# Kernel optimization log

Measured on AMD Instinct MI355X. Metric: run time of the kernel, lower is better.

The kernel has to match this reference:

```python
import jax, jax.numpy as jnp
import numpy as np

B, T, C = 1, 2048, 1024
H, KVH = 16, 4
D = C // H            # 64
KV = KVH * D          # 256
EPS = 1e-6
SCALE = 1.0 / np.sqrt(D)
ROPE_BASE = 10000.0


def setup_inputs() -> dict:
    key = jax.random.key(0)
    ks = jax.random.split(key, 8)
    s = 0.02
    return dict(
        x=jax.random.normal(ks[0], (B, T, C), jnp.float32),
        Wq=jax.random.normal(ks[1], (C, C), jnp.float32) * s,
        Wk=jax.random.normal(ks[2], (KV, C), jnp.float32) * s,
        Wv=jax.random.normal(ks[3], (KV, C), jnp.float32) * s,
        Wo=jax.random.normal(ks[4], (C, C), jnp.float32) * s,
        q_norm_w=jnp.ones((C,), jnp.float32),
        k_norm_w=jnp.ones((KV,), jnp.float32),
        fgate_w=jax.random.normal(ks[5], (H, C), jnp.float32) * s,
        fgate_b=jnp.zeros((H,), jnp.float32),
        weight_lambda=jax.random.normal(ks[6], (C, H), jnp.float32) * s,
    )


def _rmsnorm(x, w):
    var = jnp.mean(x * x, axis=-1, keepdims=True)
    return x * jax.lax.rsqrt(var + EPS) * w


def _rotate_half(x):
    x1, x2 = jnp.split(x, 2, axis=-1)
    return jnp.concatenate([-x2, x1], axis=-1)


def _apply_rope(q, k):
    # q: [B,H,T,D], k: [B,KVH,T,D]; position_ids = arange(T)
    inv_freq = 1.0 / (ROPE_BASE ** (jnp.arange(0, D, 2, dtype=jnp.float32) / D))
    freqs = jnp.outer(jnp.arange(T, dtype=jnp.float32), inv_freq)  # [T, D/2]
    emb = jnp.concatenate([freqs, freqs], axis=-1)                 # [T, D]
    cos = jnp.cos(emb)[None, None]                                  # [1,1,T,D]
    sin = jnp.sin(emb)[None, None]
    return q * cos + _rotate_half(q) * sin, k * cos + _rotate_half(k) * sin


def _forward(x, Wq, Wk, Wv, Wo, q_norm_w, k_norm_w, fgate_w, fgate_b, weight_lambda):
    q = _rmsnorm(x @ Wq.T, q_norm_w)          # [B,T,C]
    k = _rmsnorm(x @ Wk.T, k_norm_w)          # [B,T,KV]
    v = x @ Wv.T                              # [B,T,KV]
    q = q.reshape(B, T, H, D).transpose(0, 2, 1, 3)     # [B,H,T,D]
    k = k.reshape(B, T, KVH, D).transpose(0, 2, 1, 3)   # [B,KVH,T,D]
    v = v.reshape(B, T, KVH, D).transpose(0, 2, 1, 3)
    q, k = _apply_rope(q, k)
    # GQA: repeat_interleave kv heads
    g = H // KVH
    k = jnp.repeat(k, g, axis=1)              # [B,H,T,D]
    v = jnp.repeat(v, g, axis=1)
    # Forgetting gate (FoX): log f_t per head, with elu-based lambda scaling
    lam = jax.nn.elu(x @ weight_lambda) + 1.0            # [B,T,H]
    logit = (x @ fgate_w.T + fgate_b) * lam              # [B,T,H]
    log_f = (jax.nn.log_sigmoid(logit) / (lam + 1e-3)).transpose(0, 2, 1)  # [B,H,T]
    c = jnp.cumsum(log_f, axis=-1)                       # [B,H,T]
    bias = c[..., :, None] - c[..., None, :]             # [B,H,T,T]: sum_{t=j+1..i} log f_t
    scores = jnp.einsum('bhid,bhjd->bhij', q, k) * SCALE + bias
    causal = jnp.tril(jnp.ones((T, T), dtype=bool))
    scores = jnp.where(causal, scores, -jnp.inf)
    p = jax.nn.softmax(scores, axis=-1)
    y = jnp.einsum('bhij,bhjd->bhid', p, v)              # [B,H,T,D]
    y = y.transpose(0, 2, 1, 3).reshape(B, T, C)
    return y @ Wo.T


def reference(x, Wq, Wk, Wv, Wo, q_norm_w, k_norm_w, fgate_w, fgate_b, weight_lambda):
    return _forward(x, Wq, Wk, Wv, Wo, q_norm_w, k_norm_w, fgate_w, fgate_b, weight_lambda)
```

## Files before the change

kernel.cpp:

```cpp
#include <hip/hip_runtime.h>

typedef __bf16 bf16x8 __attribute__((ext_vector_type(8)));
typedef float f32x4 __attribute__((ext_vector_type(4)));

#define MFMA_BF16 __builtin_amdgcn_mfma_f32_16x16x32_bf16

static constexpr int T_ = 2048;
static constexpr int C_ = 1024;
static constexpr int H_ = 16;
static constexpr int KVH_ = 4;
static constexpr int D_ = 64;
static constexpr float INVLN2_ = 1.4426950408889634f;
static constexpr float SCALE2_ = 0.125f * 1.4426950408889634f;
static constexpr float MSHIFT_ = 10.0f;

static constexpr int UPH_ = 528;
static constexpr int NBLK_ = 1024;

__device__ inline void cvt8(__bf16* dst, const float* src) {
  float4 a = *(const float4*)src;
  float4 b = *(const float4*)(src + 4);
  bf16x8 r;
  r[0] = (__bf16)a.x; r[1] = (__bf16)a.y; r[2] = (__bf16)a.z; r[3] = (__bf16)a.w;
  r[4] = (__bf16)b.x; r[5] = (__bf16)b.y; r[6] = (__bf16)b.z; r[7] = (__bf16)b.w;
  *(bf16x8*)dst = r;
}

__global__ __launch_bounds__(256) void cvt_kernel(
    const float* __restrict__ x,  const float* __restrict__ wq,
    const float* __restrict__ wk, const float* __restrict__ wv,
    const float* __restrict__ wo, const float* __restrict__ wl,
    __bf16* __restrict__ xb,  __bf16* __restrict__ wqb,
    __bf16* __restrict__ wkb, __bf16* __restrict__ wvb,
    __bf16* __restrict__ wob, float* __restrict__ wlT,
    float* __restrict__ zbuf)
{
  size_t i8 = ((size_t)blockIdx.x * 256 + threadIdx.x) * 8;
  if (i8 < 2097152)       cvt8(xb  + i8,            x  + i8);
  else if (i8 < 3145728)  cvt8(wqb + (i8-2097152),  wq + (i8-2097152));
  else if (i8 < 3407872)  cvt8(wkb + (i8-3145728),  wk + (i8-3145728));
  else if (i8 < 3670016)  cvt8(wvb + (i8-3407872),  wv + (i8-3407872));
  else if (i8 < 4718592)  cvt8(wob + (i8-3670016),  wo + (i8-3670016));
  else if (i8 < 4734976) {
    size_t r = i8 - 4718592;
#pragma unroll
    for (int j = 0; j < 8; ++j) {
      size_t idx = r + j;
      size_t hh = idx >> 10, c = idx & 1023;
      wlT[idx] = wl[c * 16 + hh];
    }
  } else {
    size_t z = i8 - 4734976;
    if (z < 2129920) {
      float4 zz = {0.f, 0.f, 0.f, 0.f};
      *(float4*)(zbuf + z) = zz;
      *(float4*)(zbuf + z + 4) = zz;
    }
  }
}

template <int BM>
__global__ __launch_bounds__(256) void gemm_bt_kernel(
    const __bf16* __restrict__ A, int K, int N,
    const __bf16* __restrict__ B0, int e0,
    const __bf16* __restrict__ B1, int e1,
    const __bf16* __restrict__ B2,
    float* __restrict__ outF)
{
  __shared__ __bf16 la[BM * 40];
  __shared__ __bf16 lb[128 * 40];
  const int m0 = blockIdx.y * BM;
  const int n0 = blockIdx.x * 128;
  const __bf16* Bs; int nrel;
  if (n0 < e0)      { Bs = B0; nrel = n0; }
  else if (n0 < e1) { Bs = B1; nrel = n0 - e0; }
  else              { Bs = B2; nrel = n0 - e1; }
  const int tid = threadIdx.x;
  const int arow = tid >> 2, acol = (tid & 3) * 8;
  const __bf16* ap = A  + (size_t)(m0   + arow) * K + acol;
  const __bf16* bp = Bs + (size_t)(nrel + arow) * K + acol;
  const int w = tid >> 6, lane = tid & 63, lq = lane >> 4, ln = lane & 15;
  const int wm = (w >> 1) * (BM / 2), wn = (w & 1) * 64;
  constexpr int FM = BM / 32;
  f32x4 acc[FM][4] = {};
  for (int k0 = 0; k0 < K; k0 += 32) {
    bf16x8 a0 = *(const bf16x8*)(ap + k0);
    bf16x8 a1{};
    if (BM == 128) a1 = *(const bf16x8*)(ap + (size_t)64 * K + k0);
    bf16x8 b0 = *(const bf16x8*)(bp + k0);
    bf16x8 b1 = *(const bf16x8*)(bp + (size_t)64 * K + k0);
    __syncthreads();
    *(bf16x8*)(la + arow * 40 + acol) = a0;
    if (BM == 128) *(bf16x8*)(la + (arow + 64) * 40 + acol) = a1;
    *(bf16x8*)(lb + arow * 40 + acol) = b0;
    *(bf16x8*)(lb + (arow + 64) * 40 + acol) = b1;
    __syncthreads();
    bf16x8 af[FM], bfr[4];
#pragma unroll
    for (int i = 0; i < FM; ++i)
      af[i] = *(const bf16x8*)(la + (wm + i * 16 + ln) * 40 + lq * 8);
#pragma unroll
    for (int j = 0; j < 4; ++j)
      bfr[j] = *(const bf16x8*)(lb + (wn + j * 16 + ln) * 40 + lq * 8);
#pragma unroll
    for (int i = 0; i < FM; ++i)
#pragma unroll
      for (int j = 0; j < 4; ++j)
        acc[i][j] = MFMA_BF16(af[i], bfr[j], acc[i][j], 0, 0, 0);
  }
#pragma unroll
  for (int i = 0; i < FM; ++i)
#pragma unroll
    for (int j = 0; j < 4; ++j)
#pragma unroll
      for (int r = 0; r < 4; ++r) {
        int row = m0 + wm + i * 16 + lq * 4 + r;
        int col = n0 + wn + j * 16 + ln;
        outF[(size_t)row * N + col] = acc[i][j][r];
      }
}

__global__ __launch_bounds__(256) void gemmout_kernel(
    const float* __restrict__ oacc, const float* __restrict__ lsacc,
    const __bf16* __restrict__ B, float* __restrict__ outF)
{
  constexpr int K = 1024, N = 1024;
  __shared__ __bf16 la[64 * 40];
  __shared__ __bf16 lb[128 * 40];
  const int m0 = blockIdx.y * 64;
  const int n0 = blockIdx.x * 128;
  const int tid = threadIdx.x;
  const int arow = tid >> 2, acol = (tid & 3) * 8;
  const int trow = m0 + arow;
  const __bf16* bp = B + (size_t)(n0 + arow) * K + acol;
  const int w = tid >> 6, lane = tid & 63, lq = lane >> 4, ln = lane & 15;
  const int wm = (w >> 1) * 32, wn = (w & 1) * 64;
  f32x4 acc[2][4] = {};
  for (int k0 = 0; k0 < K; k0 += 32) {
    const int c = k0 + acol;
    const int hh = c >> 6, d = c & 63;
    const float* op = oacc + ((size_t)hh * T_ + trow) * D_ + d;
    float4 f0 = *(const float4*)(op);
    float4 f1 = *(const float4*)(op + 4);
    float inv = __builtin_amdgcn_rcpf(lsacc[(size_t)hh * T_ + trow]);
    bf16x8 a0;
    a0[0] = (__bf16)(f0.x * inv); a0[1] = (__bf16)(f0.y * inv);
    a0[2] = (__bf16)(f0.z * inv); a0[3] = (__bf16)(f0.w * inv);
    a0[4] = (__bf16)(f1.x * inv); a0[5] = (__bf16)(f1.y * inv);
    a0[6] = (__bf16)(f1.z * inv); a0[7] = (__bf16)(f1.w * inv);
    bf16x8 b0 = *(const bf16x8*)(bp + k0);
    bf16x8 b1 = *(const bf16x8*)(bp + (size_t)64 * K + k0);
    __syncthreads();
    *(bf16x8*)(la + arow * 40 + acol) = a0;
    *(bf16x8*)(lb + arow * 40 + acol) = b0;
    *(bf16x8*)(lb + (arow + 64) * 40 + acol) = b1;
    __syncthreads();
    bf16x8 af[2], bfr[4];
#pragma unroll
    for (int i = 0; i < 2; ++i)
      af[i] = *(const bf16x8*)(la + (wm + i * 16 + ln) * 40 + lq * 8);
#pragma unroll
    for (int j = 0; j < 4; ++j)
      bfr[j] = *(const bf16x8*)(lb + (wn + j * 16 + ln) * 40 + lq * 8);
#pragma unroll
    for (int i = 0; i < 2; ++i)
#pragma unroll
      for (int j = 0; j < 4; ++j)
        acc[i][j] = MFMA_BF16(af[i], bfr[j], acc[i][j], 0, 0, 0);
  }
#pragma unroll
  for (int i = 0; i < 2; ++i)
#pragma unroll
    for (int j = 0; j < 4; ++j)
#pragma unroll
      for (int r = 0; r < 4; ++r) {
        int row = m0 + wm + i * 16 + lq * 4 + r;
        int col = n0 + wn + j * 16 + ln;
        outF[(size_t)row * N + col] = acc[i][j][r];
      }
}

__global__ __launch_bounds__(256) void gates_kernel(
    const float* __restrict__ x, const float* __restrict__ fw,
    const float* __restrict__ fb, const float* __restrict__ wlT,
    float* __restrict__ logf)
{
  const int t0 = blockIdx.x * 4;
  const int tid = threadIdx.x, w = tid >> 6, lane = tid & 63;
  float xv[4][16];
#pragma unroll
  for (int tt = 0; tt < 4; ++tt)
#pragma unroll
    for (int i = 0; i < 16; ++i)
      xv[tt][i] = x[(size_t)(t0 + tt) * C_ + i * 64 + lane];
#pragma unroll
  for (int u = 0; u < 4; ++u) {
    int h = w * 4 + u;
    float wlr[16], fwr[16];
#pragma unroll
    for (int i = 0; i < 16; ++i) {
      wlr[i] = wlT[(size_t)h * C_ + i * 64 + lane];
      fwr[i] = fw[(size_t)h * C_ + i * 64 + lane];
    }
#pragma unroll
    for (int tt = 0; tt < 4; ++tt) {
      float s1 = 0.f, s2 = 0.f;
#pragma unroll
      for (int i = 0; i < 16; ++i) {
        s1 += xv[tt][i] * wlr[i];
        s2 += xv[tt][i] * fwr[i];
      }
      for (int m = 32; m; m >>= 1) {
        s1 += __shfl_xor(s1, m);
        s2 += __shfl_xor(s2, m);
      }
      if (lane == 0) {
        float lam = (s1 > 0.f ? s1 : expm1f(s1)) + 1.0f;
        float logit = (s2 + fb[h]) * lam;
        float ls = (logit >= 0.f) ? -log1pf(expf(-logit))
                                  : (logit - log1pf(expf(logit)));
        logf[(size_t)h * T_ + t0 + tt] = ls / (lam + 1e-3f);
      }
    }
  }
}

__global__ __launch_bounds__(256) void cumsum_kernel(
    const float* __restrict__ logf, float* __restrict__ csum)
{
  const int h = blockIdx.x;
  const int tid = threadIdx.x, lane = tid & 63, w = tid >> 6;
  __shared__ float wsum[4];
  const float* src = logf + (size_t)h * T_ + tid * 8;
  float4 a = *(const float4*)(src);
  float4 b = *(const float4*)(src + 4);
  float v[8] = {a.x, a.y, a.z, a.w, b.x, b.y, b.z, b.w};
  float t = 0.f;
#pragma unroll
  for (int j = 0; j < 8; ++j) t += v[j];
  float s = t;
#pragma unroll
  for (int d = 1; d < 64; d <<= 1) {
    float u = __shfl_up(s, d);
    if (lane >= d) s += u;
  }
  if (lane == 63) wsum[w] = s;
  __syncthreads();
  float prefix = 0.f;
#pragma unroll
  for (int ww = 0; ww < 3; ++ww)
    if (ww < w) prefix += wsum[ww];
  float run = prefix + s - t;
  float* dst = csum + (size_t)h * T_ + tid * 8;
  float4 o0, o1;
  run += v[0]; o0.x = run; run += v[1]; o0.y = run;
  run += v[2]; o0.z = run; run += v[3]; o0.w = run;
  run += v[4]; o1.x = run; run += v[5]; o1.y = run;
  run += v[6]; o1.z = run; run += v[7]; o1.w = run;
  *(float4*)dst = o0;
  *(float4*)(dst + 4) = o1;
}

__global__ __launch_bounds__(256) void normrope_kernel(
    const float* __restrict__ qkv, const float* __restrict__ qw,
    const float* __restrict__ kw, __bf16* __restrict__ qh,
    __bf16* __restrict__ kh, __bf16* __restrict__ vh)
{
  const int t = blockIdx.x, tid = threadIdx.x;
  __shared__ float qn[1024];
  __shared__ float kn[256];
  __shared__ float red[16];
  __shared__ float rc[32], rs[32];
  if (tid < 32) {
    float fr = (float)t * exp2f((float)tid * -0.41524101186404527f);
    float sn, cs;
    sincosf(fr, &sn, &cs);
    rc[tid] = cs; rs[tid] = sn;
  }
  const float* row = qkv + (size_t)t * 1536;
  float4 q4 = *(const float4*)(row + tid * 4);
  float kvl = row[1024 + tid];
  float vvl = row[1280 + tid];
  float ssq = q4.x * q4.x + q4.y * q4.y + q4.z * q4.z + q4.w * q4.w;
  float ssk = kvl * kvl;
  const int lane = tid & 63, w = tid >> 6;
  for (int m = 32; m; m >>= 1) {
    ssq += __shfl_xor(ssq, m);
    ssk += __shfl_xor(ssk, m);
  }
  if (lane == 0) { red[w] = ssq; red[8 + w] = ssk; }
  __syncthreads();
  float sq = red[0] + red[1] + red[2] + red[3];
  float sk = red[8] + red[9] + red[10] + red[11];
  float rq = rsqrtf(sq * (1.0f / 1024.f) + 1e-6f);
  float rk = rsqrtf(sk * (1.0f / 256.f) + 1e-6f);
  qn[tid * 4 + 0] = q4.x * rq * qw[tid * 4 + 0];
  qn[tid * 4 + 1] = q4.y * rq * qw[tid * 4 + 1];
  qn[tid * 4 + 2] = q4.z * rq * qw[tid * 4 + 2];
  qn[tid * 4 + 3] = q4.w * rq * qw[tid * 4 + 3];
  kn[tid] = kvl * rk * kw[tid];
  __syncthreads();
#pragma unroll
  for (int u = 0; u < 4; ++u) {
    int cidx = tid * 4 + u;
    int hh = cidx >> 6, d = cidx & 63, i = d & 31;
    float cs = rc[i], sn = rs[i];
    float val = (d < 32) ? (qn[cidx] * cs - qn[cidx + 32] * sn)
                         : (qn[cidx] * cs + qn[cidx - 32] * sn);
    qh[(size_t)hh * T_ * D_ + (size_t)t * D_ + d] = (__bf16)val;
  }
  {
    int d = tid & 63, kvhh = tid >> 6, i = d & 31;
    float cs = rc[i], sn = rs[i];
    float kval = (d < 32) ? (kn[tid] * cs - kn[tid + 32] * sn)
                          : (kn[tid] * cs + kn[tid - 32] * sn);
    kh[(size_t)kvhh * T_ * D_ + (size_t)t * D_ + d] = (__bf16)kval;
    vh[(size_t)kvhh * T_ * D_ + (size_t)t * D_ + d] = (__bf16)vvl;
  }
}

__global__ __launch_bounds__(256) void vtrans_kernel(
    const __bf16* __restrict__ vh, __bf16* __restrict__ vt)
{
  const int tb = blockIdx.x, kvh = blockIdx.y;
  __shared__ __bf16 tile[64][72];
  const int tid = threadIdx.x;
  const int r = tid >> 2, cb = (tid & 3) * 16;
  const __bf16* src = vh + (size_t)kvh * T_ * D_ + (size_t)(tb * 64 + r) * D_ + cb;
  bf16x8 v0 = *(const bf16x8*)(src);
  bf16x8 v1 = *(const bf16x8*)(src + 8);
  *(bf16x8*)(&tile[r][cb]) = v0;
  *(bf16x8*)(&tile[r][cb + 8]) = v1;
  __syncthreads();
  bf16x8 o0, o1;
#pragma unroll
  for (int j = 0; j < 8; ++j) o0[j] = tile[cb + j][r];
#pragma unroll
  for (int j = 0; j < 8; ++j) o1[j] = tile[cb + 8 + j][r];
  __bf16* dst = vt + (size_t)kvh * D_ * T_ + (size_t)r * T_ + tb * 64 + cb;
  *(bf16x8*)(dst) = o0;
  *(bf16x8*)(dst + 8) = o1;
}

__device__ inline unsigned cvtpk_bf16(float a, float b) {
  unsigned r;
  asm("v_cvt_pk_bf16_f32 %0, %1, %2" : "=v"(r) : "v"(a), "v"(b));
  return r;
}

__global__ __launch_bounds__(256, 4) void attn_kernel(
    const __bf16* __restrict__ qh, const __bf16* __restrict__ kh,
    const __bf16* __restrict__ vt, const float* __restrict__ csum,
    float* __restrict__ oacc, float* __restrict__ lsacc)
{
  const int bid = blockIdx.x;
  const int wgid = (bid & 7) * (NBLK_ / 8) + (bid >> 3);
  const int g4 = wgid >> 2, r4 = wgid & 3;
  const int u0 = g4 * 33 + (r4 ? 9 + (r4 - 1) * 8 : 0);
  const int cnt = r4 ? 8 : 9;
  __shared__ __bf16 kbuf[2][64 * 72];
  __shared__ __bf16 vbuf[2][64 * 72];
  const int tid = threadIdx.x;
  const int w = tid >> 6, lane = tid & 63, lq = lane >> 4, ln = lane & 15;
  const int srow = tid >> 2, scol = (tid & 3) * 16;
  bf16x8 ones;
#pragma unroll
  for (int j = 0; j < 8; ++j) ones[j] = (__bf16)1.0f;

  auto dec = [](int u, int& h, int& ib, int& jt) {
    h = u / UPH_;
    int uh = u - h * UPH_;
    int b = (int)((sqrtf((float)(8 * uh + 1)) - 1.f) * 0.5f);
    if (b * (b + 1) / 2 > uh) --b;
    if ((b + 1) * (b + 2) / 2 <= uh) ++b;
    ib = b; jt = uh - b * (b + 1) / 2;
  };

  int h, ib, jt;
  dec(u0, h, ib, jt);
  int kvh = h >> 2;

  bf16x8 aq0, aq1;
  float ci2;
  f32x4 o[4] = {};
  f32x4 ls = {0.f, 0.f, 0.f, 0.f};
  auto loadQ = [&](int h_, int i0_) {
    const __bf16* qp = qh + ((size_t)h_ * T_ + i0_ + w * 16 + ln) * D_;
    aq0 = *(const bf16x8*)(qp + lq * 8);
    aq1 = *(const bf16x8*)(qp + 32 + lq * 8);
    ci2 = (csum[(size_t)h_ * T_ + i0_ + w * 16 + ln] - MSHIFT_) * INVLN2_;
#pragma unroll
    for (int dd = 0; dd < 4; ++dd) o[dd] = f32x4{0.f, 0.f, 0.f, 0.f};
    ls = f32x4{0.f, 0.f, 0.f, 0.f};
  };
  loadQ(h, ib * 64);

  auto fetchRegs = [&](int kvh_, int jt_, bf16x8& k0, bf16x8& k1,
                       bf16x8& v0, bf16x8& v1) {
    const __bf16* kb = kh + (size_t)kvh_ * T_ * D_;
    const __bf16* vb = vt + (size_t)kvh_ * D_ * T_;
    k0 = *(const bf16x8*)(kb + (size_t)(jt_ * 64 + srow) * D_ + scol);
    k1 = *(const bf16x8*)(kb + (size_t)(jt_ * 64 + srow) * D_ + scol + 8);
    v0 = *(const bf16x8*)(vb + (size_t)srow * T_ + jt_ * 64 + scol);
    v1 = *(const bf16x8*)(vb + (size_t)srow * T_ + jt_ * 64 + scol + 8);
  };
  auto writeStage = [&](int cb, bf16x8 k0, bf16x8 k1, bf16x8 v0, bf16x8 v1) {
    *(bf16x8*)(kbuf[cb] + srow * 72 + scol) = k0;
    *(bf16x8*)(kbuf[cb] + srow * 72 + scol + 8) = k1;
    *(bf16x8*)(vbuf[cb] + srow * 72 + scol) = v0;
    *(bf16x8*)(vbuf[cb] + srow * 72 + scol + 8) = v1;
  };

  auto tilebody = [&](int cb, int j0, bool diag) {
    const __bf16* kt = kbuf[cb];
    const __bf16* vtt = vbuf[cb];
    __bf16* pw = kbuf[cb ^ 1] + w * 16 * 72;
    f32x4 cj2[4];
#pragma unroll
    for (int jj = 0; jj < 4; ++jj) {
      float4 c4 = *(const float4*)(csum + (size_t)h * T_ + j0 + jj * 16 + lq * 4);
      cj2[jj] = f32x4{c4.x * INVLN2_, c4.y * INVLN2_,
                      c4.z * INVLN2_, c4.w * INVLN2_};
    }
    f32x4 s[4];
    const f32x4 zf = {0.f, 0.f, 0.f, 0.f};
    __builtin_amdgcn_s_setprio(1);
#pragma unroll
    for (int jj = 0; jj < 4; ++jj) {
      bf16x8 bk0 = *(const bf16x8*)(kt + (jj * 16 + ln) * 72 + lq * 8);
      bf16x8 bk1 = *(const bf16x8*)(kt + (jj * 16 + ln) * 72 + 32 + lq * 8);
      s[jj] = MFMA_BF16(bk0, aq0, zf, 0, 0, 0);
      s[jj] = MFMA_BF16(bk1, aq1, s[jj], 0, 0, 0);
    }
    __builtin_amdgcn_s_setprio(0);
    bf16x8 bv0[4], bv1[4];
#pragma unroll
    for (int dd = 0; dd < 4; ++dd) {
      bv0[dd] = *(const bf16x8*)(vtt + (dd * 16 + ln) * 72 + lq * 8);
      bv1[dd] = *(const bf16x8*)(vtt + (dd * 16 + ln) * 72 + 32 + lq * 8);
    }
    const int qloc = w * 16 + ln;
#pragma unroll
    for (int jj = 0; jj < 4; ++jj) {
      float p[4];
#pragma unroll
      for (int r = 0; r < 4; ++r) {
        float arg = fmaf(s[jj][r], SCALE2_, ci2 - cj2[jj][r]);
        p[r] = exp2f(arg);
        if (diag && (jj * 16 + lq * 4 + r > qloc)) p[r] = 0.f;
      }
      unsigned lo = cvtpk_bf16(p[0], p[1]);
      unsigned hi = cvtpk_bf16(p[2], p[3]);
      uint2 pr; pr.x = lo; pr.y = hi;
      *(uint2*)(pw + ln * 72 + jj * 16 + lq * 4) = pr;
    }
    asm volatile("s_waitcnt lgkmcnt(0)" ::: "memory");
    bf16x8 pa0 = *(const bf16x8*)(pw + ln * 72 + lq * 8);
    bf16x8 pa1 = *(const bf16x8*)(pw + ln * 72 + 32 + lq * 8);
    __builtin_amdgcn_s_setprio(1);
    ls = MFMA_BF16(pa0, ones, ls, 0, 0, 0);
    ls = MFMA_BF16(pa1, ones, ls, 0, 0, 0);
#pragma unroll
    for (int dd = 0; dd < 4; ++dd) {
      o[dd] = MFMA_BF16(pa0, bv0[dd], o[dd], 0, 0, 0);
      o[dd] = MFMA_BF16(pa1, bv1[dd], o[dd], 0, 0, 0);
    }
    __builtin_amdgcn_s_setprio(0);
  };

  auto flush = [&]() {
    const int i0 = ib * 64;
#pragma unroll
    for (int dd = 0; dd < 4; ++dd)
#pragma unroll
      for (int r = 0; r < 4; ++r) {
        int iabs = i0 + w * 16 + lq * 4 + r;
        atomicAdd(oacc + ((size_t)h * T_ + iabs) * D_ + dd * 16 + ln,
                  o[dd][r]);
      }
    if (ln == 0) {
#pragma unroll
      for (int r = 0; r < 4; ++r)
        atomicAdd(lsacc + (size_t)h * T_ + ib * 64 + w * 16 + lq * 4 + r,
                  ls[r]);
    }
  };

  {
    bf16x8 k0, k1, v0, v1;
    fetchRegs(kvh, jt, k0, k1, v0, v1);
    writeStage(0, k0, k1, v0, v1);
  }
  __syncthreads();

  int cur = 0;
#pragma unroll 1
  for (int s = 0; s < cnt; ++s) {
    const bool last = (s == cnt - 1);
    int nh = 0, nib = 0, njt = 0;
    bf16x8 k0, k1, v0, v1;
    if (!last) {
      dec(u0 + s + 1, nh, nib, njt);
      fetchRegs(nh >> 2, njt, k0, k1, v0, v1);
    }
    tilebody(cur, jt * 64, jt == ib);
    if (!last) writeStage(cur ^ 1, k0, k1, v0, v1);
    const bool rowEnd = last || nib != ib || nh != h;
    if (rowEnd) flush();
    if (!last) {
      __syncthreads();
      if (nh != h || nib != ib) loadQ(nh, nib * 64);
      h = nh; ib = nib; jt = njt; kvh = nh >> 2;
      cur ^= 1;
    }
  }
}

extern "C" void kernel_launch(void* const* d_in, const int* in_sizes, int n_in,
                              void* d_out, int out_size, void* d_ws, size_t ws_size,
                              hipStream_t stream) {
  const float* x   = (const float*)d_in[0];
  const float* Wq  = (const float*)d_in[1];
  const float* Wk  = (const float*)d_in[2];
  const float* Wv  = (const float*)d_in[3];
  const float* Wo  = (const float*)d_in[4];
  const float* qnw = (const float*)d_in[5];
  const float* knw = (const float*)d_in[6];
  const float* fgw = (const float*)d_in[7];
  const float* fgb = (const float*)d_in[8];
  const float* wl  = (const float*)d_in[9];

  char* ws = (char*)d_ws;
  size_t off = 0;
  float*  qkv  = (float*)(ws + off);  off += (size_t)T_ * 1536 * 4;
  float*  logf = (float*)(ws + off);  off += (size_t)H_ * T_ * 4;
  float*  csum = (float*)(ws + off);  off += (size_t)H_ * T_ * 4;
  __bf16* qh   = (__bf16*)(ws + off); off += (size_t)H_ * T_ * D_ * 2;
  __bf16* kh   = (__bf16*)(ws + off); off += (size_t)KVH_ * T_ * D_ * 2;
  __bf16* vh   = (__bf16*)(ws + off); off += (size_t)KVH_ * T_ * D_ * 2;
  __bf16* vt   = (__bf16*)(ws + off); off += (size_t)KVH_ * T_ * D_ * 2;
  __bf16* xb   = (__bf16*)(ws + off); off += (size_t)T_ * C_ * 2;
  __bf16* wqb  = (__bf16*)(ws + off); off += (size_t)C_ * C_ * 2;
  __bf16* wkb  = (__bf16*)(ws + off); off += (size_t)256 * C_ * 2;
  __bf16* wvb  = (__bf16*)(ws + off); off += (size_t)256 * C_ * 2;
  __bf16* wob  = (__bf16*)(ws + off); off += (size_t)C_ * C_ * 2;
  float*  wlT  = (float*)(ws + off);  off += (size_t)H_ * C_ * 4;
  float*  oacc = (float*)(ws + off);  off += (size_t)H_ * T_ * D_ * 4;
  float*  lsacc= (float*)(ws + off);  off += (size_t)H_ * T_ * 4;

  cvt_kernel<<<3352, 256, 0, stream>>>(x, Wq, Wk, Wv, Wo, wl,
                                       xb, wqb, wkb, wvb, wob, wlT, oacc);
  gemm_bt_kernel<128><<<dim3(12, 16), 256, 0, stream>>>(
      xb, 1024, 1536, wqb, 1024, wkb, 1280, wvb, qkv);
  gates_kernel<<<T_ / 4, 256, 0, stream>>>(x, fgw, fgb, wlT, logf);
  cumsum_kernel<<<H_, 256, 0, stream>>>(logf, csum);
  normrope_kernel<<<T_, 256, 0, stream>>>(qkv, qnw, knw, qh, kh, vh);
  vtrans_kernel<<<dim3(T_ / 64, KVH_), 256, 0, stream>>>(vh, vt);
  attn_kernel<<<NBLK_, 256, 0, stream>>>(qh, kh, vt, csum, oacc, lsacc);
  gemmout_kernel<<<dim3(8, 32), 256, 0, stream>>>(
      oacc, lsacc, wob, (float*)d_out);
}
```

Baseline: 197.7 us.

## Fuse gate computation into conversion kernel and halve QKV GEMM row tile

The forgetting-gate computation moves into the conversion kernel as 512 extra blocks. Each of these blocks transposes weight_lambda into a 64KB shared-memory buffer instead of reading a global transposed copy, which drops one kernel launch and the wlT workspace. Separately, the QKV GEMM switches from 128-row to 64-row tiles, doubling its grid to 384 blocks for better CU occupancy. The 64KB static shared allocation applies to every block of the fused kernel, including the conversion-only blocks, so occupancy of the bulk conversion work may drop sharply.

```diff
diff --git a/kernel.cpp b/kernel.cpp
--- a/kernel.cpp
+++ b/kernel.cpp
@@ -26,31 +26,78 @@
   *(bf16x8*)dst = r;
 }
 
-__global__ __launch_bounds__(256) void cvt_kernel(
+__global__ __launch_bounds__(256) void cvtgates_kernel(
     const float* __restrict__ x,  const float* __restrict__ wq,
     const float* __restrict__ wk, const float* __restrict__ wv,
     const float* __restrict__ wo, const float* __restrict__ wl,
     __bf16* __restrict__ xb,  __bf16* __restrict__ wqb,
     __bf16* __restrict__ wkb, __bf16* __restrict__ wvb,
-    __bf16* __restrict__ wob, float* __restrict__ wlT,
-    float* __restrict__ zbuf)
-{
+    __bf16* __restrict__ wob, float* __restrict__ zbuf,
+    const float* __restrict__ fw, const float* __restrict__ fb,
+    float* __restrict__ logf)
+{
+  __shared__ float wlds[16 * 1024];
+  if (blockIdx.x >= 3344) {
+    const int t0 = (blockIdx.x - 3344) * 4;
+    const int tid = threadIdx.x, w = tid >> 6, lane = tid & 63;
+    const float4* wl4 = (const float4*)wl;
+#pragma unroll
+    for (int j = 0; j < 16; ++j) {
+      float4 f = wl4[j * 256 + tid];
+      int e = (j * 256 + tid) * 4;
+      int c = e >> 4, h0 = e & 15;
+      wlds[(h0 + 0) * 1024 + c] = f.x;
+      wlds[(h0 + 1) * 1024 + c] = f.y;
+      wlds[(h0 + 2) * 1024 + c] = f.z;
+      wlds[(h0 + 3) * 1024 + c] = f.w;
+    }
+    float xv[4][16];
+#pragma unroll
+    for (int tt = 0; tt < 4; ++tt)
+#pragma unroll
+      for (int i = 0; i < 16; ++i)
+        xv[tt][i] = x[(size_t)(t0 + tt) * C_ + i * 64 + lane];
+    __syncthreads();
+#pragma unroll
+    for (int u = 0; u < 4; ++u) {
+      int h = w * 4 + u;
+      float wlr[16], fwr[16];
+#pragma unroll
+      for (int i = 0; i < 16; ++i) {
+        wlr[i] = wlds[h * 1024 + i * 64 + lane];
+        fwr[i] = fw[(size_t)h * C_ + i * 64 + lane];
+      }
+#pragma unroll
+      for (int tt = 0; tt < 4; ++tt) {
+        float s1 = 0.f, s2 = 0.f;
+#pragma unroll
+        for (int i = 0; i < 16; ++i) {
+          s1 += xv[tt][i] * wlr[i];
+          s2 += xv[tt][i] * fwr[i];
+        }
+        for (int m = 32; m; m >>= 1) {
+          s1 += __shfl_xor(s1, m);
+          s2 += __shfl_xor(s2, m);
+        }
+        if (lane == 0) {
+          float lam = (s1 > 0.f ? s1 : expm1f(s1)) + 1.0f;
+          float logit = (s2 + fb[h]) * lam;
+          float ls = (logit >= 0.f) ? -log1pf(expf(-logit))
+                                    : (logit - log1pf(expf(logit)));
+          logf[(size_t)h * T_ + t0 + tt] = ls / (lam + 1e-3f);
+        }
+      }
+    }
+    return;
+  }
   size_t i8 = ((size_t)blockIdx.x * 256 + threadIdx.x) * 8;
   if (i8 < 2097152)       cvt8(xb  + i8,            x  + i8);
   else if (i8 < 3145728)  cvt8(wqb + (i8-2097152),  wq + (i8-2097152));
   else if (i8 < 3407872)  cvt8(wkb + (i8-3145728),  wk + (i8-3145728));
   else if (i8 < 3670016)  cvt8(wvb + (i8-3407872),  wv + (i8-3407872));
   else if (i8 < 4718592)  cvt8(wob + (i8-3670016),  wo + (i8-3670016));
-  else if (i8 < 4734976) {
-    size_t r = i8 - 4718592;
-#pragma unroll
-    for (int j = 0; j < 8; ++j) {
-      size_t idx = r + j;
-      size_t hh = idx >> 10, c = idx & 1023;
-      wlT[idx] = wl[c * 16 + hh];
-    }
-  } else {
-    size_t z = i8 - 4734976;
+  else {
+    size_t z = i8 - 4718592;
     if (z < 2129920) {
       float4 zz = {0.f, 0.f, 0.f, 0.f};
       *(float4*)(zbuf + z) = zz;
@@ -180,51 +227,6 @@
       }
 }
 
-__global__ __launch_bounds__(256) void gates_kernel(
-    const float* __restrict__ x, const float* __restrict__ fw,
-    const float* __restrict__ fb, const float* __restrict__ wlT,
-    float* __restrict__ logf)
-{
-  const int t0 = blockIdx.x * 4;
-  const int tid = threadIdx.x, w = tid >> 6, lane = tid & 63;
-  float xv[4][16];
-#pragma unroll
-  for (int tt = 0; tt < 4; ++tt)
-#pragma unroll
-    for (int i = 0; i < 16; ++i)
-      xv[tt][i] = x[(size_t)(t0 + tt) * C_ + i * 64 + lane];
-#pragma unroll
-  for (int u = 0; u < 4; ++u) {
-    int h = w * 4 + u;
-    float wlr[16], fwr[16];
-#pragma unroll
-    for (int i = 0; i < 16; ++i) {
-      wlr[i] = wlT[(size_t)h * C_ + i * 64 + lane];
-      fwr[i] = fw[(size_t)h * C_ + i * 64 + lane];
-    }
-#pragma unroll
-    for (int tt = 0; tt < 4; ++tt) {
-      float s1 = 0.f, s2 = 0.f;
-#pragma unroll
-      for (int i = 0; i < 16; ++i) {
-        s1 += xv[tt][i] * wlr[i];
-        s2 += xv[tt][i] * fwr[i];
-      }
-      for (int m = 32; m; m >>= 1) {
-        s1 += __shfl_xor(s1, m);
-        s2 += __shfl_xor(s2, m);
-      }
-      if (lane == 0) {
-        float lam = (s1 > 0.f ? s1 : expm1f(s1)) + 1.0f;
-        float logit = (s2 + fb[h]) * lam;
-        float ls = (logit >= 0.f) ? -log1pf(expf(-logit))
-                                  : (logit - log1pf(expf(logit)));
-        logf[(size_t)h * T_ + t0 + tt] = ls / (lam + 1e-3f);
-      }
-    }
-  }
-}
-
 __global__ __launch_bounds__(256) void cumsum_kernel(
     const float* __restrict__ logf, float* __restrict__ csum)
 {
@@ -544,15 +546,13 @@
   __bf16* wkb  = (__bf16*)(ws + off); off += (size_t)256 * C_ * 2;
   __bf16* wvb  = (__bf16*)(ws + off); off += (size_t)256 * C_ * 2;
   __bf16* wob  = (__bf16*)(ws + off); off += (size_t)C_ * C_ * 2;
-  float*  wlT  = (float*)(ws + off);  off += (size_t)H_ * C_ * 4;
   float*  oacc = (float*)(ws + off);  off += (size_t)H_ * T_ * D_ * 4;
   float*  lsacc= (float*)(ws + off);  off += (size_t)H_ * T_ * 4;
 
-  cvt_kernel<<<3352, 256, 0, stream>>>(x, Wq, Wk, Wv, Wo, wl,
-                                       xb, wqb, wkb, wvb, wob, wlT, oacc);
-  gemm_bt_kernel<128><<<dim3(12, 16), 256, 0, stream>>>(
+  cvtgates_kernel<<<3344 + 512, 256, 0, stream>>>(
+      x, Wq, Wk, Wv, Wo, wl, xb, wqb, wkb, wvb, wob, oacc, fgw, fgb, logf);
+  gemm_bt_kernel<64><<<dim3(12, 32), 256, 0, stream>>>(
       xb, 1024, 1536, wqb, 1024, wkb, 1280, wvb, qkv);
-  gates_kernel<<<T_ / 4, 256, 0, stream>>>(x, fgw, fgb, wlT, logf);
   cumsum_kernel<<<H_, 256, 0, stream>>>(logf, csum);
   normrope_kernel<<<T_, 256, 0, stream>>>(qkv, qnw, knw, qh, kh, vh);
   vtrans_kernel<<<dim3(T_ / 64, KVH_), 256, 0, stream>>>(vh, vt);
```

Measured after the change: 194.3 us. Within noise of the previous version (-1.7%).
